# Kernel tuning notes

Hardware: AMD Instinct MI355X
Metric: run time of the kernel (lower is better)

## Reference

```python
import jax, jax.numpy as jnp
import numpy as np

# sizes
N, B, NPG = 8192, 8, 1024          # total nodes, graphs, nodes per graph (equal-size graphs)
D, H, DH, L = 256, 8, 32, 2        # hidden, heads, head dim, layers
IN_C, OUT_D, E, DFF = 128, 64, 262144, 512
EPS = 1e-5


def setup_inputs() -> dict:
    key = jax.random.key(0)
    ks = jax.random.split(key, 20)
    p = lambda i, shp: jax.random.normal(ks[i], shp, jnp.float32) * 0.05
    return dict(
        x=jax.random.normal(ks[0], (N, IN_C), jnp.float32),
        edge_index=jax.random.randint(ks[1], (2, E), 0, N),
        batch=jnp.arange(N, dtype=jnp.int32) // NPG,  # sorted, equal-size graphs
        w_in=p(2, (D, IN_C)), b_in=p(3, (D,)),
        sage_wl=p(4, (L, D, D)), sage_bl=p(5, (L, D)), sage_wr=p(6, (L, D, D)),
        attn_iw=p(7, (L, 3 * D, D)), attn_ib=p(8, (L, 3 * D)),
        attn_ow=p(9, (L, D, D)), attn_ob=p(10, (L, D)),
        n1_w=jnp.ones((L, D)), n1_b=jnp.zeros((L, D)),
        n2_w=jnp.ones((L, D)), n2_b=jnp.zeros((L, D)),
        n3_w=jnp.ones((L, D)), n3_b=jnp.zeros((L, D)),
        mlp_w1=p(11, (L, DFF, D)), mlp_b1=p(12, (L, DFF)),
        mlp_w2=p(13, (L, D, DFF)), mlp_b2=p(14, (L, D)),
        bn_w=jnp.ones((L, D)), bn_b=jnp.zeros((L, D)),
        w_out=p(15, (OUT_D, D)), b_out=p(16, (OUT_D,)),
    )


def _bn(h, w, b):
    # BatchNorm1d over nodes (training-mode batch statistics, biased var)
    m = h.mean(0)
    v = jnp.mean((h - m) ** 2, axis=0)
    return (h - m) * jax.lax.rsqrt(v + EPS) * w + b


def _forward(x, edge_index, batch, w_in, b_in, sage_wl, sage_bl, sage_wr,
             attn_iw, attn_ib, attn_ow, attn_ob, n1_w, n1_b, n2_w, n2_b,
             n3_w, n3_b, mlp_w1, mlp_b1, mlp_w2, mlp_b2, bn_w, bn_b, w_out, b_out):
    src, dst = edge_index[0], edge_index[1]
    deg = jax.ops.segment_sum(jnp.ones((E,), jnp.float32), dst, num_segments=N)
    inv_deg = (1.0 / jnp.clip(deg, 1.0))[:, None]
    scale = 1.0 / np.sqrt(DH)

    h = x @ w_in.T + b_in  # in_proj Linear  [N, D]
    for l in range(L):
        # --- GPSConv: local SAGEConv (mean aggr) + residual + norm1 ---
        agg = jax.ops.segment_sum(h[src], dst, num_segments=N) * inv_deg
        loc = agg @ sage_wl[l].T + sage_bl[l] + h @ sage_wr[l].T
        loc = _bn(loc + h, n1_w[l], n1_b[l])
        # --- GPSConv: dense per-graph multi-head self-attention + residual + norm2 ---
        hd = h.reshape(B, NPG, D)  # to_dense_batch (no padding: equal graph sizes)
        qkv = hd @ attn_iw[l].T + attn_ib[l]  # [B, n, 3D]
        q, k, v = jnp.split(qkv, 3, axis=-1)
        sh = lambda t: t.reshape(B, NPG, H, DH).transpose(0, 2, 1, 3)  # [B, H, n, DH]
        a = jax.nn.softmax(jnp.einsum('bhqd,bhkd->bhqk', sh(q) * scale, sh(k)), axis=-1)
        o = jnp.einsum('bhqk,bhkd->bhqd', a, sh(v)).transpose(0, 2, 1, 3).reshape(B, NPG, D)
        o = (o @ attn_ow[l].T + attn_ob[l]).reshape(N, D)
        glob = _bn(o + h, n2_w[l], n2_b[l])
        # --- GPSConv: sum branches, MLP residual, norm3 ---
        out = loc + glob
        out = out + jax.nn.relu(out @ mlp_w1[l].T + mlp_b1[l]) @ mlp_w2[l].T + mlp_b2[l]
        out = _bn(out, n3_w[l], n3_b[l])
        # --- outer GPS: BatchNorm + relu + (dropout=eval) + residual ---
        h = h + jax.nn.relu(_bn(out, bn_w[l], bn_b[l]))
    pooled = h.reshape(B, NPG, D).mean(axis=1)  # global_mean_pool over sorted equal-size graphs
    return pooled @ w_out.T + b_out  # [B, OUT_D]


def reference(x, edge_index, batch, w_in, b_in, sage_wl, sage_bl, sage_wr,
              attn_iw, attn_ib, attn_ow, attn_ob, n1_w, n1_b, n2_w, n2_b,
              n3_w, n3_b, mlp_w1, mlp_b1, mlp_w2, mlp_b2, bn_w, bn_b, w_out, b_out):
    return _forward(x, edge_index, batch, w_in, b_in, sage_wl, sage_bl, sage_wr,
                    attn_iw, attn_ib, attn_ow, attn_ob, n1_w, n1_b, n2_w, n2_b,
                    n3_w, n3_b, mlp_w1, mlp_b1, mlp_w2, mlp_b2, bn_w, bn_b, w_out, b_out)
```

## Files before the change

kernel.cpp:

```cpp
#include <hip/hip_runtime.h>
#include <hip/hip_bf16.h>

#define N_NODES 8192
#define BGRAPH 8
#define NPG 1024
#define DIM 256
#define NH 8
#define DHEAD 32
#define NLAYERS 2
#define INC 128
#define OUTD 64
#define NEDGE 262144
#define DFF 512
#define EPS 1e-5f

typedef __attribute__((ext_vector_type(4))) float f32x4;
typedef __attribute__((ext_vector_type(8))) short s16x8;
typedef __attribute__((ext_vector_type(4))) ushort u16x4;

__device__ __forceinline__ float b2f(ushort u){
  unsigned v = ((unsigned)u) << 16;
  return __builtin_bit_cast(float, v);
}
__device__ __forceinline__ ushort f2b(float f){
  unsigned u = __builtin_bit_cast(unsigned, f);
  u += 0x7fffu + ((u >> 16) & 1u);
  return (ushort)(u >> 16);
}
__device__ __forceinline__ ushort f2b_trunc(float f){
  return (ushort)(__builtin_bit_cast(unsigned, f) >> 16);
}
__device__ __forceinline__ void gload16(const void* g, void* l){
  __builtin_amdgcn_global_load_lds(
    (const __attribute__((address_space(1))) void*)g,
    (__attribute__((address_space(3))) void*)l,
    16, 0, 0);
}

#define CX  1048576
#define CWI (CX+32768)
#define CSW (CWI+262144)
#define CIW (CSW+393216)
#define COW (CIW+131072)
#define CW1 (COW+262144)
#define CW2 (CW1+262144)
#define NCAST (CW2/256)
__global__ void k_setup(const float* __restrict__ x, const float* __restrict__ w_in,
    const float* __restrict__ wl, const float* __restrict__ wr,
    const float* __restrict__ iw, const float* __restrict__ ow,
    const float* __restrict__ w1, const float* __restrict__ w2,
    ushort* __restrict__ dst, const int* __restrict__ edst, int* __restrict__ deg){
  if(blockIdx.x >= NCAST){
    int i = (blockIdx.x - NCAST)*256 + threadIdx.x;
    int stride = 512*256;
    for(; i<NEDGE; i+=stride) atomicAdd(&deg[edst[i]], 1);
    return;
  }
  int i = blockIdx.x*256 + threadIdx.x;
  float val;
  if(i < CX)       val = x[i];
  else if(i < CWI) val = w_in[i-CX];
  else if(i < CSW){
    int j = i - CWI;
    int l = j >> 17, r = (j >> 9) & 255, k = j & 511;
    val = (k < 256) ? wl[(l<<16) + (r<<8) + k] : wr[(l<<16) + (r<<8) + (k-256)];
  }
  else if(i < CIW) val = iw[i-CSW];
  else if(i < COW) val = ow[i-CIW];
  else if(i < CW1) val = w1[i-COW];
  else             val = w2[i-CW1];
  dst[i] = f2b(val);
}

__global__ void k_scan(const int* __restrict__ deg, int* __restrict__ offs,
                       float* __restrict__ inv_deg){
  __shared__ int s[1024];
  int t = threadIdx.x;
  int base = t*8;
  int loc[8]; int acc=0;
  #pragma unroll
  for(int j=0;j<8;j++){
    int dv = deg[base+j];
    inv_deg[base+j] = 1.0f/(float)(dv>0?dv:1);
    loc[j]=acc; acc += dv;
  }
  s[t]=acc;
  __syncthreads();
  for(int d=1; d<1024; d<<=1){
    int v = (t>=d)? s[t-d] : 0;
    __syncthreads();
    if(t>=d) s[t]+=v;
    __syncthreads();
  }
  int pre = (t>0)? s[t-1] : 0;
  #pragma unroll
  for(int j=0;j<8;j++) offs[base+j] = pre + loc[j];
  if(t==1023) offs[N_NODES] = s[1023];
}
__global__ void k_fill_csr(const int* __restrict__ src, const int* __restrict__ dst,
                           const int* __restrict__ offs, int* __restrict__ cursor,
                           int* __restrict__ csr){
  int i = blockIdx.x*blockDim.x + threadIdx.x;
  int stride = gridDim.x*blockDim.x;
  for(; i<NEDGE; i+=stride){
    int d = dst[i];
    int p = atomicAdd(&cursor[d], 1);
    csr[offs[d]+p] = src[i];
  }
}

#define STAGE_AB(t, buf) do{ \
    int kt_ = (t)*64; \
    _Pragma("unroll") \
    for(int it=0; it<2; ++it){ \
      int c = (wave*2+it)*64 + lane; \
      int row = c >> 3, q = c & 7; \
      int qs = q ^ (row & 7); \
      gload16(A + (size_t)(bm+row)*lda + kt_ + qs*8, (char*)As + (buf)*8192 + (wave*2+it)*1024); \
      gload16(W + (size_t)(bn+row)*K   + kt_ + qs*8, (char*)Bs + (buf)*8192 + (wave*2+it)*1024); \
    } \
  }while(0)

#define MM_LOOP \
  f32x4 acc[2][2] = {}; \
  { const int nt = K >> 6; \
    STAGE_AB(0, 0); \
    asm volatile("s_waitcnt vmcnt(0)" ::: "memory"); \
    __builtin_amdgcn_s_barrier(); \
    int cur = 0; \
    for(int t=0; t<nt; ++t){ \
      if(t+1 < nt) STAGE_AB(t+1, cur^1); \
      _Pragma("unroll") \
      for(int kk=0; kk<2; ++kk){ \
        s16x8 af[2], bfr[2]; \
        _Pragma("unroll") \
        for(int mi=0; mi<2; ++mi){ \
          int row = wr*32 + mi*16 + l15; \
          int col = (kk*64 + l4*16) ^ ((row & 7) << 4); \
          af[mi] = *(const s16x8*)((const char*)As + cur*8192 + row*128 + col); \
        } \
        _Pragma("unroll") \
        for(int nj=0; nj<2; ++nj){ \
          int row = wc*32 + nj*16 + l15; \
          int col = (kk*64 + l4*16) ^ ((row & 7) << 4); \
          bfr[nj] = *(const s16x8*)((const char*)Bs + cur*8192 + row*128 + col); \
        } \
        _Pragma("unroll") \
        for(int mi=0; mi<2; ++mi) \
          _Pragma("unroll") \
          for(int nj=0; nj<2; ++nj) \
            acc[mi][nj] = __builtin_amdgcn_mfma_f32_16x16x32_bf16(af[mi], bfr[nj], acc[mi][nj], 0,0,0); \
      } \
      asm volatile("s_waitcnt vmcnt(0)" ::: "memory"); \
      __builtin_amdgcn_s_barrier(); \
      cur ^= 1; \
    } \
  }

template<bool RELU, bool RESID, bool RESIDB, bool BIAS, bool WF32, bool WBF, bool STATS>
__global__ __launch_bounds__(256) void k_mm(const ushort* __restrict__ A,
    const ushort* __restrict__ W, const float* __restrict__ bias,
    const float* __restrict__ resid, const ushort* __restrict__ residb,
    float* __restrict__ Cf, ushort* __restrict__ Cb,
    float* __restrict__ gS, float* __restrict__ gQ,
    int M, int Nc, int K, int lda, int ldcb)
{
  __shared__ ushort As[2*64*64];
  __shared__ ushort Bs[2*64*64];
  __shared__ float sredS[64];
  __shared__ float sredQ[64];
  const int tid = threadIdx.x;
  const int lane = tid & 63, wave = tid >> 6;
  const int l15 = lane & 15, l4 = lane >> 4;
  const int bm = blockIdx.y*64, bn = blockIdx.x*64;
  const int wr = wave >> 1, wc = wave & 1;
  MM_LOOP

  float sloc[2] = {0.f,0.f}, qloc[2] = {0.f,0.f};
  #pragma unroll
  for(int mi=0; mi<2; ++mi){
    #pragma unroll
    for(int nj=0; nj<2; ++nj){
      int col = bn + wc*32 + nj*16 + l15;
      float bv = BIAS ? bias[col] : 0.f;
      #pragma unroll
      for(int r=0; r<4; ++r){
        int row = bm + wr*32 + mi*16 + l4*4 + r;
        size_t off = (size_t)row*Nc + col;
        float v = acc[mi][nj][r] + bv;
        if(RESID)  v += resid[off];
        if(RESIDB) v += b2f(residb[off]);
        if(RELU)   v = fmaxf(v, 0.f);
        if(WF32)   Cf[off] = v;
        if(WBF)    Cb[(size_t)row*ldcb + col] = f2b(v);
        if(STATS){ sloc[nj] += v; qloc[nj] += v*v; }
      }
    }
  }
  if(STATS){
    if(tid < 64){ sredS[tid]=0.f; sredQ[tid]=0.f; }
    __syncthreads();
    int c0 = wc*32 + l15;
    atomicAdd(&sredS[c0],    sloc[0]); atomicAdd(&sredQ[c0],    qloc[0]);
    atomicAdd(&sredS[c0+16], sloc[1]); atomicAdd(&sredQ[c0+16], qloc[1]);
    __syncthreads();
    if(tid < 64){
      atomicAdd(&gS[bn+tid], sredS[tid]);
      atomicAdd(&gQ[bn+tid], sredQ[tid]);
    }
  }
}

__global__ __launch_bounds__(256) void k_agg_qkv(ushort* __restrict__ hwb,
    const int* __restrict__ offs, const int* __restrict__ csr,
    const float* __restrict__ inv_deg, const ushort* __restrict__ iwb,
    const float* __restrict__ attn_ib, ushort* __restrict__ qkvb)
{
  __shared__ __align__(16) char smem[33280];
  const int tid = threadIdx.x;
  const int lane = tid & 63, wave = tid >> 6;
  if(blockIdx.x < 2048){
    int n = blockIdx.x*4 + wave;
    int beg = offs[n], end = offs[n+1];
    f32x4 a0 = {0,0,0,0}, a1 = {0,0,0,0}, a2 = {0,0,0,0}, a3 = {0,0,0,0};
    int i = beg;
    for(; i+4<=end; i+=4){
      int j0=csr[i], j1=csr[i+1], j2=csr[i+2], j3=csr[i+3];
      u16x4 v0 = *(const u16x4*)(hwb + (size_t)j0*512 + 256 + lane*4);
      u16x4 v1 = *(const u16x4*)(hwb + (size_t)j1*512 + 256 + lane*4);
      u16x4 v2 = *(const u16x4*)(hwb + (size_t)j2*512 + 256 + lane*4);
      u16x4 v3 = *(const u16x4*)(hwb + (size_t)j3*512 + 256 + lane*4);
      #pragma unroll
      for(int c=0;c<4;c++){ a0[c]+=b2f(v0[c]); a1[c]+=b2f(v1[c]);
                            a2[c]+=b2f(v2[c]); a3[c]+=b2f(v3[c]); }
    }
    for(; i<end; ++i){
      int j0=csr[i];
      u16x4 v0 = *(const u16x4*)(hwb + (size_t)j0*512 + 256 + lane*4);
      #pragma unroll
      for(int c=0;c<4;c++) a0[c]+=b2f(v0[c]);
    }
    float inv = inv_deg[n];
    u16x4 outv;
    #pragma unroll
    for(int c=0;c<4;c++) outv[c] = f2b((a0[c]+a1[c]+a2[c]+a3[c])*inv);
    *(u16x4*)(hwb + (size_t)n*512 + lane*4) = outv;
  } else {
    int idx = blockIdx.x - 2048;
    const int bn = (idx % 12)*64, bm = (idx / 12)*64;
    const int l15 = lane & 15, l4 = lane >> 4;
    const int wr = wave >> 1, wc = wave & 1;
    const ushort* A = hwb + 256;
    const ushort* W = iwb;
    const int K = 256, lda = 512;
    ushort* As = (ushort*)smem;
    ushort* Bs = As + 8192;
    MM_LOOP
    #pragma unroll
    for(int mi=0; mi<2; ++mi){
      #pragma unroll
      for(int nj=0; nj<2; ++nj){
        int col = bn + wc*32 + nj*16 + l15;
        float bv = attn_ib[col];
        #pragma unroll
        for(int r=0; r<4; ++r){
          int row = bm + wr*32 + mi*16 + l4*4 + r;
          qkvb[(size_t)row*768 + col] = f2b(acc[mi][nj][r] + bv);
        }
      }
    }
  }
}

__global__ __launch_bounds__(256) void k_attn_sage(const ushort* __restrict__ qkv,
    ushort* __restrict__ attnO, const ushort* __restrict__ hwb,
    const ushort* __restrict__ swb, const float* __restrict__ sage_bl,
    const float* __restrict__ H, ushort* __restrict__ locB,
    float* __restrict__ gS, float* __restrict__ gQ)
{
  __shared__ __align__(16) char smem[33280];
  const int tid = threadIdx.x;
  const int lane = tid & 63, wave = tid >> 6;
  const int l15 = lane & 15;
  if(blockIdx.x < 1024){
    ushort* KsB = (ushort*)smem;
    ushort* VtB = (ushort*)smem + 6144;
    const int g = lane >> 4;
    int bid = blockIdx.x;
    int h  = bid & 7;
    int bg = (bid >> 3) & 7;
    int qc = bid >> 6;
    const int nb = bg*NPG + qc*64 + wave*16;
    const int kb = bg*NPG;

    const int rho = tid >> 2, qq = tid & 3;
    const int grp = rho >> 5, r32 = rho & 31;
    const int tt = r32 >> 4, wi = r32 & 15;
    const int jperm = grp*32 + (wi >> 2)*8 + tt*4 + (wi & 3);
    const int qs = qq ^ ((rho >> 1) & 3);

    s16x8 qf = *(const s16x8*)(qkv + (size_t)(nb + l15)*768 + h*32 + g*8);
    {
      const float scale2 = 0.2550370703637335f;
      #pragma unroll
      for(int i=0;i<8;i++) qf[i] = (short)f2b(b2f((ushort)qf[i]) * scale2);
    }
    f32x4 o0 = {0.f,0.f,0.f,0.f}, o1 = {0.f,0.f,0.f,0.f};
    float mrun = -1e30f, lrun = 0.f;

    gload16(qkv + (size_t)(kb + jperm)*768 + 256 + h*32 + qs*8, (char*)KsB + wave*1024);
    s16x8 vcur = *(const s16x8*)(qkv + (size_t)(kb + lane)*768 + 512 + h*32 + wave*8);

    for(int st=0; st<16; ++st){
      int vb = st & 1;
      int kbuf = st % 3;
      ushort* vtb = VtB + vb*2048;
      #pragma unroll
      for(int i=0;i<8;i++){
        int d = wave*8 + i;
        vtb[d*64 + (lane ^ (i<<3))] = (ushort)vcur[i];
      }
      s16x8 vnext = vcur;
      if(st+1 < 16){
        gload16(qkv + (size_t)(kb + (st+1)*64 + jperm)*768 + 256 + h*32 + qs*8,
                (char*)(KsB + ((st+1)%3)*2048) + wave*1024);
        vnext = *(const s16x8*)(qkv + (size_t)(kb + (st+1)*64 + lane)*768 + 512 + h*32 + wave*8);
      }
      asm volatile("s_waitcnt lgkmcnt(0)" ::: "memory");
      __builtin_amdgcn_s_barrier();

      const char* ksb = (const char*)(KsB + kbuf*2048);
      f32x4 sc[4];
      __builtin_amdgcn_s_setprio(1);
      #pragma unroll
      for(int q4=0; q4<4; ++q4){
        int r0 = q4*16 + l15;
        s16x8 kf = *(const s16x8*)(ksb + r0*64 + ((g*16) ^ (((r0>>1)&3)<<4)));
        f32x4 z = {0.f,0.f,0.f,0.f};
        sc[q4] = __builtin_amdgcn_mfma_f32_16x16x32_bf16(kf, qf, z, 0,0,0);
      }
      __builtin_amdgcn_s_setprio(0);

      float smax = -1e30f;
      #pragma unroll
      for(int q4=0; q4<4; ++q4)
        #pragma unroll
        for(int r=0; r<4; ++r) smax = fmaxf(smax, sc[q4][r]);
      smax = fmaxf(smax, __shfl_xor(smax, 16));
      smax = fmaxf(smax, __shfl_xor(smax, 32));

      if(!__all((int)(smax <= mrun + 8.0f))){
        float mnew = fmaxf(mrun, smax);
        float alpha = exp2f(mrun - mnew);
        lrun *= alpha;
        #pragma unroll
        for(int r=0;r<4;r++){
          float ar = __shfl(alpha, (lane & 48) | (g*4 + r), 64);
          o0[r] *= ar; o1[r] *= ar;
        }
        mrun = mnew;
      }

      float p[16];
      float ps = 0.f;
      #pragma unroll
      for(int q4=0; q4<4; ++q4)
        #pragma unroll
        for(int r=0; r<4; ++r){
          float pv = exp2f(sc[q4][r] - mrun);
          p[q4*4+r] = pv; ps += pv;
        }
      ps += __shfl_xor(ps, 16);
      ps += __shfl_xor(ps, 32);
      lrun += ps;

      s16x8 pa0, pa1;
      #pragma unroll
      for(int i=0;i<8;i++){ pa0[i] = (short)f2b_trunc(p[i]); pa1[i] = (short)f2b_trunc(p[8+i]); }

      const char* vtc = (const char*)(VtB + vb*2048);
      int colb0 = g*16, colb1 = 64 + g*16;
      int d0 = l15, d1 = l15 + 16;
      s16x8 v00 = *(const s16x8*)(vtc + d0*128 + (colb0 ^ ((d0&7)<<4)));
      s16x8 v01 = *(const s16x8*)(vtc + d1*128 + (colb0 ^ ((d1&7)<<4)));
      s16x8 v10 = *(const s16x8*)(vtc + d0*128 + (colb1 ^ ((d0&7)<<4)));
      s16x8 v11 = *(const s16x8*)(vtc + d1*128 + (colb1 ^ ((d1&7)<<4)));
      __builtin_amdgcn_s_setprio(1);
      o0 = __builtin_amdgcn_mfma_f32_16x16x32_bf16(pa0, v00, o0, 0,0,0);
      o1 = __builtin_amdgcn_mfma_f32_16x16x32_bf16(pa0, v01, o1, 0,0,0);
      o0 = __builtin_amdgcn_mfma_f32_16x16x32_bf16(pa1, v10, o0, 0,0,0);
      o1 = __builtin_amdgcn_mfma_f32_16x16x32_bf16(pa1, v11, o1, 0,0,0);
      __builtin_amdgcn_s_setprio(0);

      vcur = vnext;
    }
    float inv = 1.0f/lrun;
    #pragma unroll
    for(int r=0;r<4;r++){
      int q2 = g*4 + r;
      float ir = __shfl(inv, (lane & 48) | q2, 64);
      size_t nrow = (size_t)(nb + q2)*DIM + h*32;
      attnO[nrow + l15]      = f2b(o0[r]*ir);
      attnO[nrow + 16 + l15] = f2b(o1[r]*ir);
    }
  } else {
    int idx = blockIdx.x - 1024;
    const int bn = (idx & 3)*64, bm = (idx >> 2)*64;
    const int l4 = lane >> 4;
    const int wr = wave >> 1, wc = wave & 1;
    const ushort* A = hwb;
    const ushort* W = swb;
    const int K = 512, lda = 512;
    ushort* As = (ushort*)smem;
    ushort* Bs = As + 8192;
    float* sredS = (float*)(smem + 32768);
    float* sredQ = sredS + 64;
    MM_LOOP

    float sloc[2] = {0.f,0.f}, qloc[2] = {0.f,0.f};
    #pragma unroll
    for(int mi=0; mi<2; ++mi){
      #pragma unroll
      for(int nj=0; nj<2; ++nj){
        int col = bn + wc*32 + nj*16 + l15;
        float bv = sage_bl[col];
        #pragma unroll
        for(int r=0; r<4; ++r){
          int row = bm + wr*32 + mi*16 + l4*4 + r;
          size_t off = (size_t)row*DIM + col;
          float v = acc[mi][nj][r] + bv + H[off];
          locB[off] = f2b(v);
          sloc[nj] += v; qloc[nj] += v*v;
        }
      }
    }
    if(tid < 64){ sredS[tid]=0.f; sredQ[tid]=0.f; }
    __syncthreads();
    int c0 = wc*32 + l15;
    atomicAdd(&sredS[c0],    sloc[0]); atomicAdd(&sredQ[c0],    qloc[0]);
    atomicAdd(&sredS[c0+16], sloc[1]); atomicAdd(&sredQ[c0+16], qloc[1]);
    __syncthreads();
    if(tid < 64){
      atomicAdd(&gS[bn+tid], sredS[tid]);
      atomicAdd(&gQ[bn+tid], sredQ[tid]);
    }
  }
}

__global__ __launch_bounds__(256) void k_apply12(const ushort* __restrict__ locB,
    const ushort* __restrict__ globB, const float* __restrict__ slot,
    const float* __restrict__ n1w, const float* __restrict__ n1b,
    const float* __restrict__ n2w, const float* __restrict__ n2b,
    ushort* __restrict__ combB){
  int t = blockIdx.x*256 + threadIdx.x;
  int base = t*4;
  int d0 = base & 255;
  u16x4 lv = *(const u16x4*)(locB + base);
  u16x4 gv = *(const u16x4*)(globB + base);
  f32x4 s1 = *(const f32x4*)(slot + d0);
  f32x4 q1 = *(const f32x4*)(slot + 256 + d0);
  f32x4 s2 = *(const f32x4*)(slot + 512 + d0);
  f32x4 q2 = *(const f32x4*)(slot + 768 + d0);
  f32x4 w1v = *(const f32x4*)(n1w + d0);
  f32x4 b1v = *(const f32x4*)(n1b + d0);
  f32x4 w2v = *(const f32x4*)(n2w + d0);
  f32x4 b2v = *(const f32x4*)(n2b + d0);
  const float invn = 1.0f/N_NODES;
  u16x4 outv;
  #pragma unroll
  for(int c=0;c<4;c++){
    float m1 = s1[c]*invn, v1 = q1[c]*invn - m1*m1;
    float m2 = s2[c]*invn, v2 = q2[c]*invn - m2*m2;
    float y1 = (b2f(lv[c])-m1)*rsqrtf(v1+EPS)*w1v[c] + b1v[c];
    float y2 = (b2f(gv[c])-m2)*rsqrtf(v2+EPS)*w2v[c] + b2v[c];
    outv[c] = f2b(y1 + y2);
  }
  *(u16x4*)(combB + base) = outv;
}

__global__ __launch_bounds__(256) void k_apply3o(const ushort* __restrict__ xB,
    const float* __restrict__ slot, const float* __restrict__ n3w,
    const float* __restrict__ bw, const float* __restrict__ bb,
    float* __restrict__ H, ushort* __restrict__ hwbR){
  int t = blockIdx.x*256 + threadIdx.x;
  int base = t*4;
  int d0 = base & 255;
  int row = base >> 8;
  u16x4 xv = *(const u16x4*)(xB + base);
  f32x4 s3 = *(const f32x4*)(slot + 1024 + d0);
  f32x4 q3 = *(const f32x4*)(slot + 1280 + d0);
  f32x4 wv3 = *(const f32x4*)(n3w + d0);
  f32x4 bwv = *(const f32x4*)(bw + d0);
  f32x4 bbv = *(const f32x4*)(bb + d0);
  f32x4 hv = *(f32x4*)(H + base);
  const float invn = 1.0f/N_NODES;
  u16x4 outv;
  #pragma unroll
  for(int c=0;c<4;c++){
    float m = s3[c]*invn, var = q3[c]*invn - m*m;
    float rs = rsqrtf(var+EPS);
    float gch = rs*wv3[c];
    float rso = rsqrtf(gch*gch*var + EPS);
    float yo = (b2f(xv[c])-m)*gch*rso*bwv[c] + bbv[c];
    float h = hv[c] + fmaxf(yo, 0.f);
    hv[c] = h;
    outv[c] = f2b(h);
  }
  *(f32x4*)(H + base) = hv;
  *(u16x4*)(hwbR + (size_t)row*512 + d0) = outv;
}

__global__ void k_pool(const float* __restrict__ h, float* __restrict__ pooled){
  int b = blockIdx.x, c = blockIdx.y, d = threadIdx.x;
  int r0 = c*64;
  float s=0.f;
  for(int i=0;i<64;i++) s += h[(size_t)(b*NPG + r0 + i)*DIM + d];
  atomicAdd(&pooled[b*DIM+d], s*(1.0f/NPG));
}
__global__ void k_out(const float* __restrict__ pooled, const float* __restrict__ w_out,
                      const float* __restrict__ b_out, float* __restrict__ out){
  int t = threadIdx.x;
  if(t >= BGRAPH*OUTD) return;
  int b = t/OUTD, oc = t%OUTD;
  float s = b_out[oc];
  for(int k=0;k<DIM;k++) s += pooled[b*DIM+k]*w_out[oc*DIM+k];
  out[t] = s;
}

extern "C" void kernel_launch(void* const* d_in, const int* in_sizes, int n_in,
                              void* d_out, int out_size, void* d_ws, size_t ws_size,
                              hipStream_t stream) {
  const float* x       = (const float*)d_in[0];
  const int*   edge    = (const int*)d_in[1];
  const float* w_in    = (const float*)d_in[3];
  const float* b_in    = (const float*)d_in[4];
  const float* sage_wl = (const float*)d_in[5];
  const float* sage_bl = (const float*)d_in[6];
  const float* sage_wr = (const float*)d_in[7];
  const float* attn_iw = (const float*)d_in[8];
  const float* attn_ib = (const float*)d_in[9];
  const float* attn_ow = (const float*)d_in[10];
  const float* attn_ob = (const float*)d_in[11];
  const float* n1_w = (const float*)d_in[12];
  const float* n1_b = (const float*)d_in[13];
  const float* n2_w = (const float*)d_in[14];
  const float* n2_b = (const float*)d_in[15];
  const float* n3_w = (const float*)d_in[16];
  const float* n3_b = (const float*)d_in[17];
  const float* mlp_w1 = (const float*)d_in[18];
  const float* mlp_b1 = (const float*)d_in[19];
  const float* mlp_w2 = (const float*)d_in[20];
  const float* mlp_b2 = (const float*)d_in[21];
  const float* bn_w = (const float*)d_in[22];
  const float* bn_b = (const float*)d_in[23];
  const float* w_out = (const float*)d_in[24];
  const float* b_out = (const float*)d_in[25];

  const size_t ND = (size_t)N_NODES*DIM;
  float* ws    = (float*)d_ws;
  float* H     = ws;
  ushort* wsb   = (ushort*)(ws + ND);
  ushort* locB  = wsb;
  ushort* globB = wsb + ND;
  ushort* hwb   = wsb + 2*ND;
  ushort* qkvb  = wsb + 4*ND;
  ushort* attnOb= wsb + 7*ND;
  ushort* combb = wsb + 8*ND;
  ushort* hidb  = wsb + 9*ND;
  ushort* castb = wsb + 11*ND;
  ushort* xb     = castb;
  ushort* w_in_b = castb + CX;
  ushort* sageWb = castb + CWI;
  ushort* iw_b   = castb + CSW;
  ushort* ow_b   = castb + CIW;
  ushort* w1_b   = castb + COW;
  ushort* w2_b   = castb + CW1;
  float* mf      = (float*)(castb + CW2);
  float* inv_deg = mf;
  float* bnslots = mf + 8192;
  float* pooled  = bnslots + 3072;
  int* deg    = (int*)(pooled + 2048);
  int* cursor = deg + N_NODES;
  int* offs   = cursor + N_NODES;
  int* csr    = offs + N_NODES + 8;

  const int* esrc = edge;
  const int* edst = edge + NEDGE;

  hipMemsetAsync(bnslots, 0, (3072+2048)*sizeof(float) + 2*N_NODES*sizeof(int), stream);

  k_setup<<<NCAST+512,256,0,stream>>>(x, w_in, sage_wl, sage_wr, attn_iw,
      attn_ow, mlp_w1, mlp_w2, castb, edst, deg);
  k_scan<<<1,1024,0,stream>>>(deg, offs, inv_deg);
  k_fill_csr<<<512,256,0,stream>>>(esrc, edst, offs, cursor, csr);

  k_mm<false,false,false,true,true,true,false><<<dim3(4,128),256,0,stream>>>(
      xb, w_in_b, b_in, nullptr, nullptr, H, hwb+256, nullptr, nullptr,
      N_NODES, DIM, INC, INC, 512);

  for(int l=0; l<NLAYERS; ++l){
    const ushort* swb = sageWb + (size_t)l*131072;
    const ushort* iwb = iw_b + (size_t)l*196608;
    const ushort* owb = ow_b + (size_t)l*65536;
    const ushort* w1b = w1_b + (size_t)l*131072;
    const ushort* w2b = w2_b + (size_t)l*131072;
    float* slot = bnslots + (size_t)l*1536;

    k_agg_qkv<<<3584,256,0,stream>>>(hwb, offs, csr, inv_deg, iwb,
        attn_ib + l*3*DIM, qkvb);

    k_attn_sage<<<1536,256,0,stream>>>(qkvb, attnOb, hwb, swb,
        sage_bl + l*DIM, H, locB, slot, slot+256);

    k_mm<false,true,false,true,false,true,true><<<dim3(4,128),256,0,stream>>>(
        attnOb, owb, attn_ob + l*DIM, H, nullptr, nullptr, globB, slot+512, slot+768,
        N_NODES, DIM, DIM, DIM, DIM);

    k_apply12<<<2048,256,0,stream>>>(locB, globB, slot,
        n1_w + l*DIM, n1_b + l*DIM, n2_w + l*DIM, n2_b + l*DIM, combb);

    k_mm<true,false,false,true,false,true,false><<<dim3(8,128),256,0,stream>>>(
        combb, w1b, mlp_b1 + l*DFF, nullptr, nullptr, nullptr, hidb,
        nullptr, nullptr, N_NODES, DFF, DIM, DIM, 512);
    k_mm<false,false,true,true,false,true,true><<<dim3(4,128),256,0,stream>>>(
        hidb, w2b, mlp_b2 + l*DIM, nullptr, combb, nullptr, globB,
        slot+1024, slot+1280, N_NODES, DIM, 512, 512, DIM);

    k_apply3o<<<2048,256,0,stream>>>(globB, slot, n3_w + l*DIM,
        bn_w + l*DIM, bn_b + l*DIM, H, hwb+256);
  }

  k_pool<<<dim3(BGRAPH, NPG/64),256,0,stream>>>(H, pooled);
  k_out<<<1,512,0,stream>>>(pooled, w_out, b_out, (float*)d_out);
}
```

Measured before the change: 282.0 us.

## Fuse CSR fill with input projection and single-buffer GEMM tiles in fused kernels

Merges the CSR fill kernel and the input-projection GEMM into one launch, with separate block ranges doing each job, which removes a launch and lets the two overlap. The GEMM halves inside the fused agg/qkv and attn/sage kernels now use a single-buffered staging loop, cutting their shared memory (33KB to 16–21KB). The aim is higher occupancy for the aggregation and attention blocks that share those kernels. The cost is that the GEMM blocks lose their global-to-LDS prefetch overlap and take an extra barrier per k-step.

```diff
diff --git a/kernel.cpp b/kernel.cpp
--- a/kernel.cpp
+++ b/kernel.cpp
@@ -97,17 +97,6 @@
   for(int j=0;j<8;j++) offs[base+j] = pre + loc[j];
   if(t==1023) offs[N_NODES] = s[1023];
 }
-__global__ void k_fill_csr(const int* __restrict__ src, const int* __restrict__ dst,
-                           const int* __restrict__ offs, int* __restrict__ cursor,
-                           int* __restrict__ csr){
-  int i = blockIdx.x*blockDim.x + threadIdx.x;
-  int stride = gridDim.x*blockDim.x;
-  for(; i<NEDGE; i+=stride){
-    int d = dst[i];
-    int p = atomicAdd(&cursor[d], 1);
-    csr[offs[d]+p] = src[i];
-  }
-}
 
 #define STAGE_AB(t, buf) do{ \
     int kt_ = (t)*64; \
@@ -121,6 +110,29 @@
     } \
   }while(0)
 
+#define MM_COMPUTE(BUFOFF) \
+      _Pragma("unroll") \
+      for(int kk=0; kk<2; ++kk){ \
+        s16x8 af[2], bfr[2]; \
+        _Pragma("unroll") \
+        for(int mi=0; mi<2; ++mi){ \
+          int row = wr*32 + mi*16 + l15; \
+          int col = (kk*64 + l4*16) ^ ((row & 7) << 4); \
+          af[mi] = *(const s16x8*)((const char*)As + (BUFOFF) + row*128 + col); \
+        } \
+        _Pragma("unroll") \
+        for(int nj=0; nj<2; ++nj){ \
+          int row = wc*32 + nj*16 + l15; \
+          int col = (kk*64 + l4*16) ^ ((row & 7) << 4); \
+          bfr[nj] = *(const s16x8*)((const char*)Bs + (BUFOFF) + row*128 + col); \
+        } \
+        _Pragma("unroll") \
+        for(int mi=0; mi<2; ++mi) \
+          _Pragma("unroll") \
+          for(int nj=0; nj<2; ++nj) \
+            acc[mi][nj] = __builtin_amdgcn_mfma_f32_16x16x32_bf16(af[mi], bfr[nj], acc[mi][nj], 0,0,0); \
+      }
+
 #define MM_LOOP \
   f32x4 acc[2][2] = {}; \
   { const int nt = K >> 6; \
@@ -130,30 +142,22 @@
     int cur = 0; \
     for(int t=0; t<nt; ++t){ \
       if(t+1 < nt) STAGE_AB(t+1, cur^1); \
-      _Pragma("unroll") \
-      for(int kk=0; kk<2; ++kk){ \
-        s16x8 af[2], bfr[2]; \
-        _Pragma("unroll") \
-        for(int mi=0; mi<2; ++mi){ \
-          int row = wr*32 + mi*16 + l15; \
-          int col = (kk*64 + l4*16) ^ ((row & 7) << 4); \
-          af[mi] = *(const s16x8*)((const char*)As + cur*8192 + row*128 + col); \
-        } \
-        _Pragma("unroll") \
-        for(int nj=0; nj<2; ++nj){ \
-          int row = wc*32 + nj*16 + l15; \
-          int col = (kk*64 + l4*16) ^ ((row & 7) << 4); \
-          bfr[nj] = *(const s16x8*)((const char*)Bs + cur*8192 + row*128 + col); \
-        } \
-        _Pragma("unroll") \
-        for(int mi=0; mi<2; ++mi) \
-          _Pragma("unroll") \
-          for(int nj=0; nj<2; ++nj) \
-            acc[mi][nj] = __builtin_amdgcn_mfma_f32_16x16x32_bf16(af[mi], bfr[nj], acc[mi][nj], 0,0,0); \
-      } \
+      MM_COMPUTE(cur*8192) \
       asm volatile("s_waitcnt vmcnt(0)" ::: "memory"); \
       __builtin_amdgcn_s_barrier(); \
       cur ^= 1; \
+    } \
+  }
+
+#define MM_LOOP_SB \
+  f32x4 acc[2][2] = {}; \
+  { const int nt = K >> 6; \
+    for(int t=0; t<nt; ++t){ \
+      __syncthreads(); \
+      STAGE_AB(t, 0); \
+      asm volatile("s_waitcnt vmcnt(0)" ::: "memory"); \
+      __builtin_amdgcn_s_barrier(); \
+      MM_COMPUTE(0) \
     } \
   }
 
@@ -211,12 +215,58 @@
   }
 }
 
+__global__ __launch_bounds__(256) void k_fill_inproj(const int* __restrict__ src,
+    const int* __restrict__ dst, const int* __restrict__ offs,
+    int* __restrict__ cursor, int* __restrict__ csr,
+    const ushort* __restrict__ xb, const ushort* __restrict__ w_in_b,
+    const float* __restrict__ b_in, float* __restrict__ H,
+    ushort* __restrict__ hwb)
+{
+  __shared__ __align__(16) char smem[16384];
+  const int tid = threadIdx.x;
+  if(blockIdx.x < 512){
+    int i = blockIdx.x*256 + tid;
+    for(; i<NEDGE; i+=512*256){
+      int d = dst[i];
+      int p = atomicAdd(&cursor[d], 1);
+      csr[offs[d]+p] = src[i];
+    }
+  } else {
+    int idx = blockIdx.x - 512;
+    const int lane = tid & 63, wave = tid >> 6;
+    const int l15 = lane & 15, l4 = lane >> 4;
+    const int bn = (idx & 3)*64, bm = (idx >> 2)*64;
+    const int wr = wave >> 1, wc = wave & 1;
+    const ushort* A = xb;
+    const ushort* W = w_in_b;
+    const int K = INC, lda = INC;
+    ushort* As = (ushort*)smem;
+    ushort* Bs = As + 4096;
+    MM_LOOP_SB
+    #pragma unroll
+    for(int mi=0; mi<2; ++mi){
+      #pragma unroll
+      for(int nj=0; nj<2; ++nj){
+        int col = bn + wc*32 + nj*16 + l15;
+        float bv = b_in[col];
+        #pragma unroll
+        for(int r=0; r<4; ++r){
+          int row = bm + wr*32 + mi*16 + l4*4 + r;
+          float v = acc[mi][nj][r] + bv;
+          H[(size_t)row*DIM + col] = v;
+          hwb[(size_t)row*512 + 256 + col] = f2b(v);
+        }
+      }
+    }
+  }
+}
+
 __global__ __launch_bounds__(256) void k_agg_qkv(ushort* __restrict__ hwb,
     const int* __restrict__ offs, const int* __restrict__ csr,
     const float* __restrict__ inv_deg, const ushort* __restrict__ iwb,
     const float* __restrict__ attn_ib, ushort* __restrict__ qkvb)
 {
-  __shared__ __align__(16) char smem[33280];
+  __shared__ __align__(16) char smem[16384];
   const int tid = threadIdx.x;
   const int lane = tid & 63, wave = tid >> 6;
   if(blockIdx.x < 2048){
@@ -254,8 +304,8 @@
     const ushort* W = iwb;
     const int K = 256, lda = 512;
     ushort* As = (ushort*)smem;
-    ushort* Bs = As + 8192;
-    MM_LOOP
+    ushort* Bs = As + 4096;
+    MM_LOOP_SB
     #pragma unroll
     for(int mi=0; mi<2; ++mi){
       #pragma unroll
@@ -278,7 +328,7 @@
     const float* __restrict__ H, ushort* __restrict__ locB,
     float* __restrict__ gS, float* __restrict__ gQ)
 {
-  __shared__ __align__(16) char smem[33280];
+  __shared__ __align__(16) char smem[20992];
   const int tid = threadIdx.x;
   const int lane = tid & 63, wave = tid >> 6;
   const int l15 = lane & 15;
@@ -412,10 +462,10 @@
     const ushort* W = swb;
     const int K = 512, lda = 512;
     ushort* As = (ushort*)smem;
-    ushort* Bs = As + 8192;
-    float* sredS = (float*)(smem + 32768);
+    ushort* Bs = As + 4096;
+    float* sredS = (float*)(smem + 16384);
     float* sredQ = sredS + 64;
-    MM_LOOP
+    MM_LOOP_SB
 
     float sloc[2] = {0.f,0.f}, qloc[2] = {0.f,0.f};
     #pragma unroll
@@ -592,11 +642,9 @@
   k_setup<<<NCAST+512,256,0,stream>>>(x, w_in, sage_wl, sage_wr, attn_iw,
       attn_ow, mlp_w1, mlp_w2, castb, edst, deg);
   k_scan<<<1,1024,0,stream>>>(deg, offs, inv_deg);
-  k_fill_csr<<<512,256,0,stream>>>(esrc, edst, offs, cursor, csr);
-
-  k_mm<false,false,false,true,true,true,false><<<dim3(4,128),256,0,stream>>>(
-      xb, w_in_b, b_in, nullptr, nullptr, H, hwb+256, nullptr, nullptr,
-      N_NODES, DIM, INC, INC, 512);
+
+  k_fill_inproj<<<1024,256,0,stream>>>(esrc, edst, offs, cursor, csr,
+      xb, w_in_b, b_in, H, hwb);
 
   for(int l=0; l<NLAYERS; ++l){
     const ushort* swb = sageWb + (size_t)l*131072;
```

Result: faster. 265.9 us (-5.7%).
